# Performance work log

Measured on AMD Instinct MI355X. Metric: run time of the kernel, lower is better.

## Reference

```python
import jax, jax.numpy as jnp
import numpy as np

B, T, C, H = 4, 1024, 1024, 16
DH = C // H  # 64


def l1_cdist(a, b, chunk):
    """L1 pairwise distances. a: [..., M, D], b: [..., N, D] -> [..., M, N].
    Scans over feature-dim chunks to avoid a [..., M, N, D] blowup."""
    D = a.shape[-1]
    nc = D // chunk
    a_r = jnp.moveaxis(a.reshape(a.shape[:-1] + (nc, chunk)), -2, 0)  # [nc, ..., M, c]
    b_r = jnp.moveaxis(b.reshape(b.shape[:-1] + (nc, chunk)), -2, 0)  # [nc, ..., N, c]
    init = jnp.zeros(jnp.broadcast_shapes(a.shape[:-2], b.shape[:-2]) + (a.shape[-2], b.shape[-2]), a.dtype)
    def step(acc, ab):
        ac, bc = ab
        return acc + jnp.abs(ac[..., :, None, :] - bc[..., None, :, :]).sum(-1), None
    return jax.lax.scan(step, init, (a_r, b_r))[0]


def sq_cdist(a, b):
    """Squared L2 pairwise distances via GEMM. a: [..., M, D], b: [..., N, D]."""
    aa = jnp.sum(a * a, -1)[..., :, None]
    bb = jnp.sum(b * b, -1)[..., None, :]
    ab = jnp.einsum('...md,...nd->...mn', a, b)
    return jnp.maximum(aa + bb - 2.0 * ab, 0.0)


def delta_linear(x, W, gain):
    """ProxyDeltaLinear: distance-based linear projection. x: [B,T,Din], W: [Dout,Din], gain: [Dout]."""
    Bx, Tx, Din = x.shape
    xa = jnp.tanh(x).reshape(-1, Din)          # [B*T, Din]
    wa = jnp.tanh(W)                           # [Dout, Din]
    l1m = jax.lax.stop_gradient(l1_cdist(xa, wa, 16)) / Din
    l2m = sq_cdist(xa, wa) / Din
    # straight-through: forward value uses l1_mean, gradient flows through l2_sq_mean
    dist = jax.lax.stop_gradient(l1m - l2m) + l2m
    out = (1.0 - dist).reshape(Bx, Tx, -1)
    return (out - 0.5) * gain                  # gain broadcasts over last dim


def reference(x, wq_w, wq_gain, wk_w, wk_gain, wv_w, wv_gain, wo_w, wo_b, gamma, rho):
    q = delta_linear(x, wq_w, wq_gain).reshape(B, T, H, DH).transpose(0, 2, 1, 3)  # [B,H,T,DH]
    k = delta_linear(x, wk_w, wk_gain).reshape(B, T, H, DH).transpose(0, 2, 1, 3)
    v = delta_linear(x, wv_w, wv_gain).reshape(B, T, H, DH).transpose(0, 2, 1, 3)

    l1m = jax.lax.stop_gradient(l1_cdist(q, k, 2)) / DH   # [B,H,T,T]
    l2m = sq_cdist(q, k) / DH
    dist = jax.lax.stop_gradient(l1m - l2m) + l2m

    g = jax.nn.softplus(gamma).reshape(1, H, 1, 1) + 1e-4
    r = jax.nn.softplus(rho).reshape(1, H, 1, 1) + 1e-4
    base = 1.0 / (1.0 + g * dist)
    w = base ** r
    probs = w / (jnp.sum(w, -1, keepdims=True) + 1e-6)

    out = jnp.einsum('bhqk,bhkd->bhqd', probs, v)         # [B,H,T,DH]
    out = out.transpose(0, 2, 1, 3).reshape(B, T, C)
    return out @ wo_w.T + wo_b


def setup_inputs():
    key = jax.random.key(0)
    ks = jax.random.split(key, 5)
    p = lambda kk, shape: jax.random.normal(kk, shape, jnp.float32) * 0.02
    return {
        "x": jax.random.normal(ks[0], (B, T, C), jnp.float32),
        "wq_w": p(ks[1], (C, C)), "wq_gain": jnp.full((C,), 2.0, jnp.float32),
        "wk_w": p(ks[2], (C, C)), "wk_gain": jnp.full((C,), 2.0, jnp.float32),
        "wv_w": p(ks[3], (C, C)), "wv_gain": jnp.full((C,), 2.0, jnp.float32),
        "wo_w": p(ks[4], (C, C)), "wo_b": jnp.zeros((C,), jnp.float32),
        "gamma": jnp.ones((H,), jnp.float32), "rho": jnp.full((H,), 2.0, jnp.float32),
    }
```

## Files before the change

### kernel.cpp

```cpp
#include <hip/hip_runtime.h>
#include <math.h>

namespace {
constexpr int NB  = 4;
constexpr int NT  = 1024;
constexpr int NC  = 1024;
constexpr int NH  = 16;
constexpr int MT  = NB * NT;
}

typedef _Float16 f16x8 __attribute__((ext_vector_type(8)));
typedef float f32x4 __attribute__((ext_vector_type(4)));
typedef int i32x4 __attribute__((ext_vector_type(4)));

__device__ __forceinline__ unsigned sad8(unsigned a, unsigned b, unsigned c) {
  unsigned d;
  asm("v_sad_u8 %0, %1, %2, %3" : "=v"(d) : "v"(a), "v"(b), "v"(c));
  return d;
}

__device__ __forceinline__ unsigned short f16u(float x) {
  _Float16 h = (_Float16)x;
  return __builtin_bit_cast(unsigned short, h);
}

__global__ __launch_bounds__(256) void k_prep(const float* __restrict__ x,
                                              const float* __restrict__ wq,
                                              const float* __restrict__ wk,
                                              const float* __restrict__ wv,
                                              const float* __restrict__ wo,
                                              unsigned* __restrict__ sgnx,
                                              unsigned* __restrict__ wi8,
                                              float* __restrict__ sumax,
                                              unsigned short* __restrict__ woh) {
  const int bid = blockIdx.x;
  const int tid = threadIdx.x;
  if (bid < 2048) {
    int i8o = bid * 256 + tid;
    const float4* in4 = reinterpret_cast<const float4*>(x);
    float4 v0 = in4[2 * i8o], v1 = in4[2 * i8o + 1];
    float t[8] = {v0.x, v0.y, v0.z, v0.w, v1.x, v1.y, v1.z, v1.w};
    unsigned b[8];
    float s = 0.0f;
#pragma unroll
    for (int j = 0; j < 8; ++j) {
      float tv = tanhf(t[j]);
      s += fabsf(tv);
      b[j] = (tv >= 0.0f) ? 0x01u : 0xFFu;
    }
    uint2 o = {b[0] | (b[1] << 8) | (b[2] << 16) | (b[3] << 24),
               b[4] | (b[5] << 8) | (b[6] << 16) | (b[7] << 24)};
    reinterpret_cast<uint2*>(sgnx)[i8o] = o;
#pragma unroll
    for (int off = 32; off > 0; off >>= 1) s += __shfl_down(s, off, 64);
    __shared__ float ws[4];
    if ((tid & 63) == 0) ws[tid >> 6] = s;
    __syncthreads();
    if (tid == 0) {
      sumax[2 * bid]     = ws[0] + ws[1];
      sumax[2 * bid + 1] = ws[2] + ws[3];
    }
  } else if (bid < 3584) {
    const float* in;
    int local;
    if (bid < 2560)      { in = wq; local = bid - 2048; }
    else if (bid < 3072) { in = wk; local = bid - 2560; }
    else                 { in = wv; local = bid - 3072; }
    unsigned* out = wi8 + ((bid < 2560) ? 0 : (bid < 3072) ? (1024 * 256) : (2048 * 256));
    int i8o = local * 256 + tid;
    const float4* in4 = reinterpret_cast<const float4*>(in);
    float4 v0 = in4[2 * i8o], v1 = in4[2 * i8o + 1];
    float t[8] = {v0.x, v0.y, v0.z, v0.w, v1.x, v1.y, v1.z, v1.w};
    unsigned q[8];
#pragma unroll
    for (int j = 0; j < 8; ++j) {
      int qi = __float2int_rn(tanhf(t[j]) * 1024.0f);
      q[j] = (unsigned)qi & 255u;
    }
    uint2 o = {q[0] | (q[1] << 8) | (q[2] << 16) | (q[3] << 24),
               q[4] | (q[5] << 8) | (q[6] << 16) | (q[7] << 24)};
    reinterpret_cast<uint2*>(out)[i8o] = o;
  } else {
    int i = (bid - 3584) * 256 + tid;
    const float4* in4 = reinterpret_cast<const float4*>(wo);
    float4 v0 = in4[2 * i], v1 = in4[2 * i + 1];
    ushort4 o0 = {f16u(v0.x), f16u(v0.y), f16u(v0.z), f16u(v0.w)};
    ushort4 o1 = {f16u(v1.x), f16u(v1.y), f16u(v1.z), f16u(v1.w)};
    reinterpret_cast<ushort4*>(woh)[2 * i] = o0;
    reinterpret_cast<ushort4*>(woh)[2 * i + 1] = o1;
  }
}

__global__ __launch_bounds__(256, 2) void k_signproj(const unsigned* __restrict__ sgnx,
                                                     const unsigned* __restrict__ wi8,
                                                     const float* __restrict__ sumax,
                                                     const float* __restrict__ g0,
                                                     const float* __restrict__ g1,
                                                     const float* __restrict__ g2,
                                                     unsigned* __restrict__ qq,
                                                     unsigned* __restrict__ kq,
                                                     unsigned short* __restrict__ vh) {
  __shared__ unsigned Ash[128][36];
  __shared__ unsigned Bsh[128][36];

  const int tid = threadIdx.x;
  const int n0 = blockIdx.x * 128;
  const int m0 = blockIdx.y * 128;
  const int lane = tid & 63;
  const int wvI = tid >> 6;
  const int wr = wvI >> 1, wc = wvI & 1;
  const int lr = lane & 15, lq = lane >> 4;

  i32x4 acc[4][4] = {};

  const unsigned* A = sgnx + (size_t)m0 * 256;
  const unsigned* Bm = wi8 + (size_t)n0 * 256;

  for (int ks = 0; ks < 8; ++ks) {
    __syncthreads();
#pragma unroll
    for (int p = 0; p < 4; ++p) {
      int idx = tid + p * 256;
      int r = idx >> 3;
      int q4 = (idx & 7) * 4;
      *reinterpret_cast<uint4*>(&Ash[r][q4]) =
          *reinterpret_cast<const uint4*>(A + (size_t)r * 256 + ks * 32 + q4);
      *reinterpret_cast<uint4*>(&Bsh[r][q4]) =
          *reinterpret_cast<const uint4*>(Bm + (size_t)r * 256 + ks * 32 + q4);
    }
    __syncthreads();

#pragma unroll
    for (int kk = 0; kk < 2; ++kk) {
      i32x4 af[4], bf[4];
#pragma unroll
      for (int f = 0; f < 4; ++f) {
        uint4 au = *reinterpret_cast<const uint4*>(&Ash[wr * 64 + f * 16 + lr][kk * 16 + lq * 4]);
        af[f] = __builtin_bit_cast(i32x4, au);
        uint4 bu = *reinterpret_cast<const uint4*>(&Bsh[wc * 64 + f * 16 + lr][kk * 16 + lq * 4]);
        bf[f] = __builtin_bit_cast(i32x4, bu);
      }
#pragma unroll
      for (int fm = 0; fm < 4; ++fm)
#pragma unroll
        for (int fn = 0; fn < 4; ++fn)
          acc[fm][fn] = __builtin_amdgcn_mfma_i32_16x16x64_i8(af[fm], bf[fn], acc[fm][fn], 0, 0, 0);
    }
  }

  const int z = n0 >> 10;
  const int nloc = n0 & 1023;
  const int hl = nloc >> 6;
  const int bI = m0 >> 10;
  const int tloc0 = (m0 & 1023) + wr * 64;
  const float* G = (z == 0) ? g0 : ((z == 1) ? g1 : g2);
  const int h = hl + wc;

  float sx[4][4];
#pragma unroll
  for (int fm = 0; fm < 4; ++fm) {
    float4 sv = *reinterpret_cast<const float4*>(sumax + m0 + wr * 64 + fm * 16 + lq * 4);
    sx[fm][0] = sv.x; sx[fm][1] = sv.y; sx[fm][2] = sv.z; sx[fm][3] = sv.w;
  }

  if (z < 2) {
    unsigned* dst = (z == 0) ? qq : kq;
    const int sh = (lr & 3) * 8;
#pragma unroll
    for (int fn = 0; fn < 4; ++fn) {
      float gn = G[nloc + wc * 64 + fn * 16 + lr];
      int txw = (fn * 16 + lr) >> 2;
#pragma unroll
      for (int fm = 0; fm < 4; ++fm) {
#pragma unroll
        for (int reg = 0; reg < 4; ++reg) {
          float accf = (float)acc[fm][fn][reg];
          float dist = (sx[fm][reg] - accf * (1.0f / 1024.0f)) * (1.0f / 1024.0f);
          float val = (0.5f - dist) * gn;
          unsigned p = ((unsigned)fminf(fmaxf(fmaf(val, 64.0f, 128.5f), 0.0f), 255.0f)) << sh;
          p |= __shfl_xor(p, 1, 64);
          p |= __shfl_xor(p, 2, 64);
          if ((lr & 3) == 0) {
            int t = tloc0 + fm * 16 + lq * 4 + reg;
            dst[(((size_t)(bI * NH + h)) * NT + t) * 16 + txw] = p;
          }
        }
      }
    }
  } else {
#pragma unroll
    for (int fn = 0; fn < 4; ++fn) {
      int dh = fn * 16 + lr;
      float gn = G[nloc + wc * 64 + dh];
#pragma unroll
      for (int fm = 0; fm < 4; ++fm) {
        int t0 = tloc0 + fm * 16 + lq * 4;
        ushort4 o;
#pragma unroll
        for (int reg = 0; reg < 4; ++reg) {
          float accf = (float)acc[fm][fn][reg];
          float dist = (sx[fm][reg] - accf * (1.0f / 1024.0f)) * (1.0f / 1024.0f);
          float val = (0.5f - dist) * gn;
          ((unsigned short*)&o)[reg] = f16u(val);
        }
        *reinterpret_cast<ushort4*>(vh + ((size_t)(bI * NH + h) * 64 + dh) * NT + t0) = o;
      }
    }
  }
}

__global__ __launch_bounds__(256, 2) void k_attn5(const unsigned* __restrict__ qq,
                                                  const unsigned* __restrict__ kq,
                                                  const unsigned short* __restrict__ vh,
                                                  const float* __restrict__ gamma,
                                                  const float* __restrict__ rho,
                                                  unsigned short* __restrict__ att_h) {
  const int qt = blockIdx.x;
  const int h  = blockIdx.y;
  const int b  = blockIdx.z;

  __shared__ unsigned Qs[16][132];
  __shared__ unsigned Ks[16][132];
  __shared__ unsigned Vt[64][68];
  __shared__ unsigned Ws[128][72];
  __shared__ float Inv[128];

  const int tid = threadIdx.x;
  const int lane = tid & 63;
  const int lr = lane & 15, lq = lane >> 4;
  const int w32 = (tid >> 6) * 32;
  const int ty = tid >> 4;
  const int tx = tid & 15;

  const float g  = log1pf(expf(gamma[h])) + 1e-4f;
  const float rr = log1pf(expf(rho[h])) + 1e-4f;
  const float gs = g * (1.0f / (64.0f * 64.0f));

  const unsigned* qbase = qq + (((size_t)(b * NH + h)) * NT + qt * 128) * 16;
#pragma unroll
  for (int p = 0; p < 2; ++p) {
    int idx = tid + p * 256;
    int r = idx >> 2;
    int c4 = (idx & 3) * 4;
    uint4 v = *reinterpret_cast<const uint4*>(qbase + (size_t)r * 16 + c4);
    Qs[c4 + 0][r] = v.x; Qs[c4 + 1][r] = v.y;
    Qs[c4 + 2][r] = v.z; Qs[c4 + 3][r] = v.w;
  }

  f32x4 acc[2][4] = {};
  float wsum[8] = {0.f, 0.f, 0.f, 0.f, 0.f, 0.f, 0.f, 0.f};

  const unsigned* kbh = kq + (((size_t)(b * NH + h)) * NT) * 16;
  const unsigned* v32 = reinterpret_cast<const unsigned*>(vh + ((size_t)(b * NH + h) * 64) * NT);

  for (int kt = 0; kt < 8; ++kt) {
    __syncthreads();
    const unsigned* kbase = kbh + (size_t)(kt * 128) * 16;
#pragma unroll
    for (int p = 0; p < 2; ++p) {
      int idx = tid + p * 256;
      int r = idx >> 2;
      int c4 = (idx & 3) * 4;
      uint4 v = *reinterpret_cast<const uint4*>(kbase + (size_t)r * 16 + c4);
      int cc = ((r & 7) < 4) ? ((r >> 3) * 4 + (r & 3)) : (64 + (r >> 3) * 4 + (r & 3));
      Ks[c4 + 0][cc] = v.x; Ks[c4 + 1][cc] = v.y;
      Ks[c4 + 2][cc] = v.z; Ks[c4 + 3][cc] = v.w;
    }
#pragma unroll
    for (int p = 0; p < 4; ++p) {
      int idx = tid + p * 256;
      int d = idx >> 4;
      int q4 = (idx & 15) * 4;
      uint4 v = *reinterpret_cast<const uint4*>(v32 + (size_t)d * 512 + kt * 64 + q4);
      *reinterpret_cast<uint4*>(&Vt[d][q4]) = v;
    }
    __syncthreads();

    unsigned dl[8][8] = {};
#pragma unroll 4
    for (int du = 0; du < 16; ++du) {
      uint4 q0 = *reinterpret_cast<const uint4*>(&Qs[du][ty * 8]);
      uint4 q1 = *reinterpret_cast<const uint4*>(&Qs[du][ty * 8 + 4]);
      uint4 k0 = *reinterpret_cast<const uint4*>(&Ks[du][tx * 4]);
      uint4 k1 = *reinterpret_cast<const uint4*>(&Ks[du][64 + tx * 4]);
      unsigned qa[8] = {q0.x, q0.y, q0.z, q0.w, q1.x, q1.y, q1.z, q1.w};
      unsigned ka[8] = {k0.x, k0.y, k0.z, k0.w, k1.x, k1.y, k1.z, k1.w};
#pragma unroll
      for (int i = 0; i < 8; ++i)
#pragma unroll
        for (int j = 0; j < 8; ++j) dl[i][j] = sad8(qa[i], ka[j], dl[i][j]);
    }

#pragma unroll
    for (int i = 0; i < 8; ++i) {
      int qrow = ty * 8 + i;
      float w0[8];
#pragma unroll
      for (int j = 0; j < 8; ++j)
        w0[j] = exp2f(-rr * log2f(fmaf(gs, (float)dl[i][j], 1.0f)));
      wsum[i] += ((w0[0] + w0[1]) + (w0[2] + w0[3])) + ((w0[4] + w0[5]) + (w0[6] + w0[7]));
      uint4 pk;
      pk.x = (unsigned)f16u(w0[0]) | ((unsigned)f16u(w0[1]) << 16);
      pk.y = (unsigned)f16u(w0[2]) | ((unsigned)f16u(w0[3]) << 16);
      pk.z = (unsigned)f16u(w0[4]) | ((unsigned)f16u(w0[5]) << 16);
      pk.w = (unsigned)f16u(w0[6]) | ((unsigned)f16u(w0[7]) << 16);
      *reinterpret_cast<uint4*>(&Ws[qrow][(tx * 4) ^ ((qrow & 1) << 2)]) = pk;
    }
    __syncthreads();

#pragma unroll
    for (int kk = 0; kk < 4; ++kk) {
      f16x8 af[2];
#pragma unroll
      for (int fm = 0; fm < 2; ++fm) {
        int r = w32 + fm * 16 + lr;
        uint4 au = *reinterpret_cast<const uint4*>(&Ws[r][(kk * 16 + lq * 4) ^ ((r & 1) << 2)]);
        af[fm] = __builtin_bit_cast(f16x8, au);
      }
#pragma unroll
      for (int nt = 0; nt < 4; ++nt) {
        uint4 bu = *reinterpret_cast<const uint4*>(&Vt[nt * 16 + lr][kk * 16 + lq * 4]);
        f16x8 bf = __builtin_bit_cast(f16x8, bu);
#pragma unroll
        for (int fm = 0; fm < 2; ++fm)
          acc[fm][nt] = __builtin_amdgcn_mfma_f32_16x16x32_f16(af[fm], bf, acc[fm][nt], 0, 0, 0);
      }
    }
  }

#pragma unroll
  for (int i = 0; i < 8; ++i) {
    float s = wsum[i];
    s += __shfl_xor(s, 1, 64);
    s += __shfl_xor(s, 2, 64);
    s += __shfl_xor(s, 4, 64);
    s += __shfl_xor(s, 8, 64);
    if (lr == 0) Inv[w32 + lq * 8 + i] = 1.0f / (s + 1e-6f);
  }
  __syncthreads();

#pragma unroll
  for (int fm = 0; fm < 2; ++fm) {
    float iv[4];
#pragma unroll
    for (int r = 0; r < 4; ++r) iv[r] = Inv[w32 + fm * 16 + lq * 4 + r];
    const size_t rowbase = (size_t)(b * NT + qt * 128 + w32 + fm * 16 + lq * 4);
    const int colbase = h * 64 + lr;
#pragma unroll
    for (int nt = 0; nt < 4; ++nt)
#pragma unroll
      for (int r = 0; r < 4; ++r)
        att_h[(rowbase + r) * NC + colbase + nt * 16] = f16u(acc[fm][nt][r] * iv[r]);
  }
}

__global__ __launch_bounds__(256) void k_gemm16(const unsigned short* __restrict__ A,
                                                const unsigned short* __restrict__ Bw,
                                                const float* __restrict__ bias,
                                                float* __restrict__ Out) {
  __shared__ unsigned Ash[128 * 20];
  __shared__ unsigned Bsh[128 * 20];

  const int tid = threadIdx.x;
  const int m0 = blockIdx.y * 128;
  const int n0 = blockIdx.x * 128;
  const int lane = tid & 63;
  const int wv = tid >> 6;
  const int wr = wv >> 1, wc = wv & 1;
  const int lr = lane & 15, lq = lane >> 4;

  f32x4 acc[4][4] = {};

  const unsigned* A32 = reinterpret_cast<const unsigned*>(A);
  const unsigned* B32 = reinterpret_cast<const unsigned*>(Bw);

  for (int ks = 0; ks < 32; ++ks) {
    __syncthreads();
#pragma unroll
    for (int p = 0; p < 2; ++p) {
      int idx = tid + p * 256;
      int r = idx >> 2, q = idx & 3;
      uint4 av = *reinterpret_cast<const uint4*>(A32 + (size_t)(m0 + r) * 512 + ks * 16 + q * 4);
      *reinterpret_cast<uint4*>(&Ash[r * 20 + q * 4]) = av;
      uint4 bv = *reinterpret_cast<const uint4*>(B32 + (size_t)(n0 + r) * 512 + ks * 16 + q * 4);
      *reinterpret_cast<uint4*>(&Bsh[r * 20 + q * 4]) = bv;
    }
    __syncthreads();

    f16x8 af[4], bf[4];
#pragma unroll
    for (int f = 0; f < 4; ++f) {
      uint4 au = *reinterpret_cast<const uint4*>(&Ash[(wr * 64 + f * 16 + lr) * 20 + lq * 4]);
      af[f] = __builtin_bit_cast(f16x8, au);
      uint4 bu = *reinterpret_cast<const uint4*>(&Bsh[(wc * 64 + f * 16 + lr) * 20 + lq * 4]);
      bf[f] = __builtin_bit_cast(f16x8, bu);
    }
#pragma unroll
    for (int fm = 0; fm < 4; ++fm)
#pragma unroll
      for (int fn = 0; fn < 4; ++fn)
        acc[fm][fn] = __builtin_amdgcn_mfma_f32_16x16x32_f16(af[fm], bf[fn], acc[fm][fn], 0, 0, 0);
  }

#pragma unroll
  for (int fn = 0; fn < 4; ++fn) {
    int col = n0 + wc * 64 + fn * 16 + lr;
    float bb = bias[col];
#pragma unroll
    for (int fm = 0; fm < 4; ++fm) {
      int rowb = m0 + wr * 64 + fm * 16 + lq * 4;
#pragma unroll
      for (int r = 0; r < 4; ++r)
        Out[(size_t)(rowb + r) * NC + col] = acc[fm][fn][r] + bb;
    }
  }
}

extern "C" void kernel_launch(void* const* d_in, const int* in_sizes, int n_in,
                              void* d_out, int out_size, void* d_ws, size_t ws_size,
                              hipStream_t stream) {
  (void)in_sizes; (void)n_in; (void)out_size; (void)ws_size;
  const float* x     = (const float*)d_in[0];
  const float* wq_w  = (const float*)d_in[1];
  const float* wq_g  = (const float*)d_in[2];
  const float* wk_w  = (const float*)d_in[3];
  const float* wk_g  = (const float*)d_in[4];
  const float* wv_w  = (const float*)d_in[5];
  const float* wv_g  = (const float*)d_in[6];
  const float* wo_w  = (const float*)d_in[7];
  const float* wo_b  = (const float*)d_in[8];
  const float* gamma = (const float*)d_in[9];
  const float* rho   = (const float*)d_in[10];
  float* out = (float*)d_out;

  unsigned* sgnx = (unsigned*)d_ws;
  unsigned* wi8  = sgnx + (size_t)MT * 256;
  float* sumax   = (float*)(wi8 + 3072ull * 256);
  unsigned* qqhm = (unsigned*)(sumax + MT);
  unsigned* kqhm = qqhm + (size_t)NB * NH * NT * 16;
  unsigned short* vhdm = (unsigned short*)(kqhm + (size_t)NB * NH * NT * 16);
  unsigned short* atth = vhdm + (size_t)NB * NH * 64 * NT;
  unsigned short* woh  = atth + (size_t)MT * NC;

  k_prep<<<4096, 256, 0, stream>>>(x, wq_w, wk_w, wv_w, wo_w, sgnx, wi8, sumax, woh);

  k_signproj<<<dim3(3072 / 128, MT / 128), 256, 0, stream>>>(sgnx, wi8, sumax,
                                                             wq_g, wk_g, wv_g,
                                                             qqhm, kqhm, vhdm);

  k_attn5<<<dim3(NT / 128, NH, NB), 256, 0, stream>>>(qqhm, kqhm, vhdm, gamma, rho, atth);

  k_gemm16<<<dim3(NC / 128, MT / 128, 1), 256, 0, stream>>>(atth, woh, wo_b, out);
}
```

Baseline: 142.4 us.

## Halve attention query tile and register-prefetch next K/V tile

The attention kernel now processes 64 query rows per block instead of 128, which doubles the grid and shrinks shared memory and per-thread accumulators so three blocks can be resident per CU. Each thread now computes an 8x4 SAD tile, and the row-sum reduction gains one more shuffle stage. K and V tiles for the next iteration are loaded into registers while the current tile is being computed, hiding global load latency. In exchange, every K/V tile is reloaded twice as many times across blocks, and the ratio of compute to LDS traffic per block drops.

```diff
diff --git a/kernel.cpp b/kernel.cpp
--- a/kernel.cpp
+++ b/kernel.cpp
@@ -209,7 +209,7 @@
   }
 }
 
-__global__ __launch_bounds__(256, 2) void k_attn5(const unsigned* __restrict__ qq,
+__global__ __launch_bounds__(256, 3) void k_attn6(const unsigned* __restrict__ qq,
                                                   const unsigned* __restrict__ kq,
                                                   const unsigned short* __restrict__ vh,
                                                   const float* __restrict__ gamma,
@@ -219,111 +219,114 @@
   const int h  = blockIdx.y;
   const int b  = blockIdx.z;
 
-  __shared__ unsigned Qs[16][132];
+  __shared__ unsigned Qs[16][68];
   __shared__ unsigned Ks[16][132];
   __shared__ unsigned Vt[64][68];
-  __shared__ unsigned Ws[128][72];
-  __shared__ float Inv[128];
+  __shared__ unsigned Ws[64][68];
+  __shared__ float Inv[64];
 
   const int tid = threadIdx.x;
   const int lane = tid & 63;
   const int lr = lane & 15, lq = lane >> 4;
-  const int w32 = (tid >> 6) * 32;
-  const int ty = tid >> 4;
-  const int tx = tid & 15;
+  const int w16 = (tid >> 6) * 16;
+  const int ty = tid >> 5;
+  const int tx = tid & 31;
 
   const float g  = log1pf(expf(gamma[h])) + 1e-4f;
   const float rr = log1pf(expf(rho[h])) + 1e-4f;
   const float gs = g * (1.0f / (64.0f * 64.0f));
 
-  const unsigned* qbase = qq + (((size_t)(b * NH + h)) * NT + qt * 128) * 16;
-#pragma unroll
-  for (int p = 0; p < 2; ++p) {
-    int idx = tid + p * 256;
-    int r = idx >> 2;
-    int c4 = (idx & 3) * 4;
+  const unsigned* qbase = qq + (((size_t)(b * NH + h)) * NT + qt * 64) * 16;
+  {
+    int r = tid >> 2;
+    int c4 = (tid & 3) * 4;
     uint4 v = *reinterpret_cast<const uint4*>(qbase + (size_t)r * 16 + c4);
     Qs[c4 + 0][r] = v.x; Qs[c4 + 1][r] = v.y;
     Qs[c4 + 2][r] = v.z; Qs[c4 + 3][r] = v.w;
   }
 
-  f32x4 acc[2][4] = {};
+  f32x4 acc[4] = {};
   float wsum[8] = {0.f, 0.f, 0.f, 0.f, 0.f, 0.f, 0.f, 0.f};
 
   const unsigned* kbh = kq + (((size_t)(b * NH + h)) * NT) * 16;
   const unsigned* v32 = reinterpret_cast<const unsigned*>(vh + ((size_t)(b * NH + h) * 64) * NT);
 
+  const int kr0 = tid >> 2;
+  const int kc4 = (tid & 3) * 4;
+  const int vd = tid >> 4;
+  const int vq4 = (tid & 15) * 4;
+
+  uint4 kreg[2], vreg[4];
+#pragma unroll
+  for (int p = 0; p < 2; ++p)
+    kreg[p] = *reinterpret_cast<const uint4*>(kbh + (size_t)(kr0 + p * 64) * 16 + kc4);
+#pragma unroll
+  for (int p = 0; p < 4; ++p)
+    vreg[p] = *reinterpret_cast<const uint4*>(v32 + (size_t)(vd + p * 16) * 512 + vq4);
+
   for (int kt = 0; kt < 8; ++kt) {
     __syncthreads();
-    const unsigned* kbase = kbh + (size_t)(kt * 128) * 16;
 #pragma unroll
     for (int p = 0; p < 2; ++p) {
-      int idx = tid + p * 256;
-      int r = idx >> 2;
-      int c4 = (idx & 3) * 4;
-      uint4 v = *reinterpret_cast<const uint4*>(kbase + (size_t)r * 16 + c4);
+      int r = kr0 + p * 64;
       int cc = ((r & 7) < 4) ? ((r >> 3) * 4 + (r & 3)) : (64 + (r >> 3) * 4 + (r & 3));
-      Ks[c4 + 0][cc] = v.x; Ks[c4 + 1][cc] = v.y;
-      Ks[c4 + 2][cc] = v.z; Ks[c4 + 3][cc] = v.w;
-    }
-#pragma unroll
-    for (int p = 0; p < 4; ++p) {
-      int idx = tid + p * 256;
-      int d = idx >> 4;
-      int q4 = (idx & 15) * 4;
-      uint4 v = *reinterpret_cast<const uint4*>(v32 + (size_t)d * 512 + kt * 64 + q4);
-      *reinterpret_cast<uint4*>(&Vt[d][q4]) = v;
-    }
-    __syncthreads();
-
-    unsigned dl[8][8] = {};
-#pragma unroll 4
+      Ks[kc4 + 0][cc] = kreg[p].x; Ks[kc4 + 1][cc] = kreg[p].y;
+      Ks[kc4 + 2][cc] = kreg[p].z; Ks[kc4 + 3][cc] = kreg[p].w;
+    }
+#pragma unroll
+    for (int p = 0; p < 4; ++p)
+      *reinterpret_cast<uint4*>(&Vt[vd + p * 16][vq4]) = vreg[p];
+    __syncthreads();
+
+    if (kt < 7) {
+      const unsigned* kbase = kbh + (size_t)((kt + 1) * 128) * 16;
+#pragma unroll
+      for (int p = 0; p < 2; ++p)
+        kreg[p] = *reinterpret_cast<const uint4*>(kbase + (size_t)(kr0 + p * 64) * 16 + kc4);
+#pragma unroll
+      for (int p = 0; p < 4; ++p)
+        vreg[p] = *reinterpret_cast<const uint4*>(v32 + (size_t)(vd + p * 16) * 512 + (kt + 1) * 64 + vq4);
+    }
+
+    const int kbase_col = ((tx & 1) << 6) + (tx >> 1) * 4;
+    unsigned dl[8][4] = {};
+#pragma unroll 8
     for (int du = 0; du < 16; ++du) {
       uint4 q0 = *reinterpret_cast<const uint4*>(&Qs[du][ty * 8]);
       uint4 q1 = *reinterpret_cast<const uint4*>(&Qs[du][ty * 8 + 4]);
-      uint4 k0 = *reinterpret_cast<const uint4*>(&Ks[du][tx * 4]);
-      uint4 k1 = *reinterpret_cast<const uint4*>(&Ks[du][64 + tx * 4]);
+      uint4 kv = *reinterpret_cast<const uint4*>(&Ks[du][kbase_col]);
       unsigned qa[8] = {q0.x, q0.y, q0.z, q0.w, q1.x, q1.y, q1.z, q1.w};
-      unsigned ka[8] = {k0.x, k0.y, k0.z, k0.w, k1.x, k1.y, k1.z, k1.w};
+      unsigned ka[4] = {kv.x, kv.y, kv.z, kv.w};
 #pragma unroll
       for (int i = 0; i < 8; ++i)
 #pragma unroll
-        for (int j = 0; j < 8; ++j) dl[i][j] = sad8(qa[i], ka[j], dl[i][j]);
+        for (int j = 0; j < 4; ++j) dl[i][j] = sad8(qa[i], ka[j], dl[i][j]);
     }
 
 #pragma unroll
     for (int i = 0; i < 8; ++i) {
       int qrow = ty * 8 + i;
-      float w0[8];
-#pragma unroll
-      for (int j = 0; j < 8; ++j)
+      float w0[4];
+#pragma unroll
+      for (int j = 0; j < 4; ++j)
         w0[j] = exp2f(-rr * log2f(fmaf(gs, (float)dl[i][j], 1.0f)));
-      wsum[i] += ((w0[0] + w0[1]) + (w0[2] + w0[3])) + ((w0[4] + w0[5]) + (w0[6] + w0[7]));
-      uint4 pk;
-      pk.x = (unsigned)f16u(w0[0]) | ((unsigned)f16u(w0[1]) << 16);
-      pk.y = (unsigned)f16u(w0[2]) | ((unsigned)f16u(w0[3]) << 16);
-      pk.z = (unsigned)f16u(w0[4]) | ((unsigned)f16u(w0[5]) << 16);
-      pk.w = (unsigned)f16u(w0[6]) | ((unsigned)f16u(w0[7]) << 16);
-      *reinterpret_cast<uint4*>(&Ws[qrow][(tx * 4) ^ ((qrow & 1) << 2)]) = pk;
+      wsum[i] += (w0[0] + w0[1]) + (w0[2] + w0[3]);
+      uint2 pk = {(unsigned)f16u(w0[0]) | ((unsigned)f16u(w0[1]) << 16),
+                  (unsigned)f16u(w0[2]) | ((unsigned)f16u(w0[3]) << 16)};
+      *reinterpret_cast<uint2*>(&Ws[qrow][(tx * 2) ^ ((qrow & 1) << 2)]) = pk;
     }
     __syncthreads();
 
 #pragma unroll
     for (int kk = 0; kk < 4; ++kk) {
-      f16x8 af[2];
-#pragma unroll
-      for (int fm = 0; fm < 2; ++fm) {
-        int r = w32 + fm * 16 + lr;
-        uint4 au = *reinterpret_cast<const uint4*>(&Ws[r][(kk * 16 + lq * 4) ^ ((r & 1) << 2)]);
-        af[fm] = __builtin_bit_cast(f16x8, au);
-      }
+      int r = w16 + lr;
+      uint4 au = *reinterpret_cast<const uint4*>(&Ws[r][(kk * 16 + lq * 4) ^ ((r & 1) << 2)]);
+      f16x8 af = __builtin_bit_cast(f16x8, au);
 #pragma unroll
       for (int nt = 0; nt < 4; ++nt) {
         uint4 bu = *reinterpret_cast<const uint4*>(&Vt[nt * 16 + lr][kk * 16 + lq * 4]);
         f16x8 bf = __builtin_bit_cast(f16x8, bu);
-#pragma unroll
-        for (int fm = 0; fm < 2; ++fm)
-          acc[fm][nt] = __builtin_amdgcn_mfma_f32_16x16x32_f16(af[fm], bf, acc[fm][nt], 0, 0, 0);
+        acc[nt] = __builtin_amdgcn_mfma_f32_16x16x32_f16(af, bf, acc[nt], 0, 0, 0);
       }
     }
   }
@@ -335,22 +338,22 @@
     s += __shfl_xor(s, 2, 64);
     s += __shfl_xor(s, 4, 64);
     s += __shfl_xor(s, 8, 64);
-    if (lr == 0) Inv[w32 + lq * 8 + i] = 1.0f / (s + 1e-6f);
+    s += __shfl_xor(s, 16, 64);
+    if (tx == 0) Inv[ty * 8 + i] = 1.0f / (s + 1e-6f);
   }
   __syncthreads();
 
-#pragma unroll
-  for (int fm = 0; fm < 2; ++fm) {
+  {
     float iv[4];
 #pragma unroll
-    for (int r = 0; r < 4; ++r) iv[r] = Inv[w32 + fm * 16 + lq * 4 + r];
-    const size_t rowbase = (size_t)(b * NT + qt * 128 + w32 + fm * 16 + lq * 4);
+    for (int r = 0; r < 4; ++r) iv[r] = Inv[w16 + lq * 4 + r];
+    const size_t rowbase = (size_t)(b * NT + qt * 64 + w16 + lq * 4);
     const int colbase = h * 64 + lr;
 #pragma unroll
     for (int nt = 0; nt < 4; ++nt)
 #pragma unroll
       for (int r = 0; r < 4; ++r)
-        att_h[(rowbase + r) * NC + colbase + nt * 16] = f16u(acc[fm][nt][r] * iv[r]);
+        att_h[(rowbase + r) * NC + colbase + nt * 16] = f16u(acc[nt][r] * iv[r]);
   }
 }
 
@@ -448,7 +451,7 @@
                                                              wq_g, wk_g, wv_g,
                                                              qqhm, kqhm, vhdm);
 
-  k_attn5<<<dim3(NT / 128, NH, NB), 256, 0, stream>>>(qqhm, kqhm, vhdm, gamma, rho, atth);
+  k_attn6<<<dim3(NT / 64, NH, NB), 256, 0, stream>>>(qqhm, kqhm, vhdm, gamma, rho, atth);
 
   k_gemm16<<<dim3(NC / 128, MT / 128, 1), 256, 0, stream>>>(atth, woh, wo_b, out);
 }
```

New measurement: 155.3 us. +9.1%, slower.
